# Kernel optimization log

Hardware: AMD Instinct MI355X
Metric: run time of the kernel (lower is better)

## Reference

```python
import jax, jax.numpy as jnp
import numpy as np

SIZE = 7
SIGMA = 1.5
K1 = 0.01
K2 = 0.03
DATA_RANGE = 2.0
NP_ = SIZE * SIZE
COV_NORM = NP_ / (NP_ - 1)
PAD = SIZE // 2


def _gaussian_window(size=SIZE, sigma=SIGMA, channels=1):
    x = np.arange(size) - size // 2
    g = np.exp(-x**2 / (2.0 * sigma**2))[None, :]
    g = (g.T @ g)
    g = g / g.sum()
    w = np.tile(g[None, None], (channels, 1, 1, 1))  # [C,1,size,size]
    return jnp.asarray(w, dtype=jnp.float32)


def _dwconv(x, w):
    # depthwise conv2d, zero padding PAD, stride 1; x: [N,C,H,W], w: [C,1,k,k]
    c = x.shape[1]
    return jax.lax.conv_general_dilated(
        x, w, window_strides=(1, 1), padding=[(PAD, PAD), (PAD, PAD)],
        dimension_numbers=('NCHW', 'OIHW', 'NCHW'), feature_group_count=c)


def setup_inputs() -> dict:
    key = jax.random.key(0)
    k1, k2 = jax.random.split(key)
    X = jax.random.uniform(k1, (64, 1, 320, 320), dtype=jnp.float32)
    Y = jax.random.uniform(k2, (64, 1, 320, 320), dtype=jnp.float32)
    window = _gaussian_window()
    return {"X": X, "Y": Y, "window": window}


def reference(X, Y, window):
    C1 = (K1 * DATA_RANGE) ** 2
    C2 = (K2 * DATA_RANGE) ** 2
    mux = _dwconv(X, window)
    muy = _dwconv(Y, window)
    mux_sq = mux * mux
    muy_sq = muy * muy
    muxy = mux * muy
    sigmax_sq = (_dwconv(X * X, window) - mux_sq) * COV_NORM
    sigmay_sq = (_dwconv(Y * Y, window) - muy_sq) * COV_NORM
    sigmaxy = (_dwconv(X * Y, window) - muxy) * COV_NORM
    ssim_map = ((2 * muxy + C1) * (2 * sigmaxy + C2)) / \
               ((mux_sq + muy_sq + C1) * (sigmax_sq + sigmay_sq + C2))
    return 1.0 - ssim_map.mean()
```

## Files before the change

kernel.cpp:

```cpp
#include <hip/hip_runtime.h>
#include <math.h>


#define WI 320
#define HI 320
#define NI 64
#define TWO 58
#define GXD 6
#define RPB 32
#define ITERS 8
#define GYD 10
#define NBLK (GXD * GYD * NI)
#define NPIX ((double)NI * WI * HI)

typedef float v4 __attribute__((ext_vector_type(4)));

struct W7 { float w[7]; };

__device__ __forceinline__ void issue_loads(
    const float* __restrict__ Xn, const float* __restrict__ Yn,
    int gx, bool xok, int ybase, float (&xr)[10], float (&yr)[10])
{
#pragma unroll
    for (int j = 0; j < 10; ++j) {
        const int gy  = ybase + j;
        const bool ok = xok && ((unsigned)gy < (unsigned)HI);
        float xv = 0.f, yv = 0.f;
        if (ok) { const int idx = gy * WI + gx; xv = Xn[idx]; yv = Yn[idx]; }
        xr[j] = xv; yr[j] = yv;
    }
}

__device__ __forceinline__ float compute_strip(
    const W7& wv, float* __restrict__ vb,
    const float (&xr)[10], const float (&yr)[10], int lane, int maxc)
{
    float acc[5][4];
#pragma unroll
    for (int ch = 0; ch < 5; ++ch)
#pragma unroll
        for (int r = 0; r < 4; ++r) acc[ch][r] = 0.f;
#pragma unroll
    for (int j = 0; j < 10; ++j) {
        const float xv = xr[j], yv = yr[j];
        const float pxx = xv * xv, pyy = yv * yv, pxy = xv * yv;
#pragma unroll
        for (int r = 0; r < 4; ++r) {
            const int d = j - r;
            if (d >= 0 && d < 7) {
                const float w = wv.w[d];
                acc[0][r] += w * xv;
                acc[1][r] += w * yv;
                acc[2][r] += w * pxx;
                acc[3][r] += w * pyy;
                acc[4][r] += w * pxy;
            }
        }
    }
#pragma unroll
    for (int ch = 0; ch < 5; ++ch)
#pragma unroll
        for (int r = 0; r < 4; ++r)
            vb[ch * 256 + r * 64 + lane] = acc[ch][r];

    __builtin_amdgcn_wave_barrier();

    const int row = lane >> 4;
    const int xg  = (lane & 15) << 2;
    const float C1 = 0.0004f, C2 = 0.0036f, COVN = 49.f / 48.f;

    float m[4][5];
#pragma unroll
    for (int j = 0; j < 4; ++j)
#pragma unroll
        for (int ch = 0; ch < 5; ++ch) m[j][ch] = 0.f;
#pragma unroll
    for (int ch = 0; ch < 5; ++ch) {
        const v4* p = (const v4*)&vb[ch * 256 + row * 64 + xg];
        v4 a = p[0], b = p[1], c = p[2];
        float f[12] = {a.x,a.y,a.z,a.w, b.x,b.y,b.z,b.w, c.x,c.y,c.z,c.w};
#pragma unroll
        for (int j = 0; j < 4; ++j) {
            float s = 0.f;
#pragma unroll
            for (int d = 0; d < 7; ++d) s += wv.w[d] * f[j + d];
            m[j][ch] = s;
        }
    }
    float lsum = 0.f;
#pragma unroll
    for (int j = 0; j < 4; ++j) {
        const float mx = m[j][0], my = m[j][1];
        const float mxsq = mx * mx;
        const float mysq = my * my;
        const float mxy  = mx * my;
        const float vx   = (m[j][2] - mxsq) * COVN;
        const float vy   = (m[j][3] - mysq) * COVN;
        const float vxy  = (m[j][4] - mxy)  * COVN;
        const float num  = (2.f * mxy + C1) * (2.f * vxy + C2);
        const float den  = (mxsq + mysq + C1) * (vx + vy + C2);
        lsum += (xg + j < maxc) ? num * __builtin_amdgcn_rcpf(den) : 0.f;
    }
    return lsum;
}

__global__ __launch_bounds__(64) void ssim_kernel(
    const float* __restrict__ X, const float* __restrict__ Y,
    W7 wv, float* __restrict__ partial)
{
    __shared__ __align__(16) float vbuf[5 * 4 * 64 + 16];

    const int lane = threadIdx.x;
    const int x0   = blockIdx.x * TWO;
    const int y0   = blockIdx.y * RPB;
    const float* __restrict__ Xn = X + (size_t)blockIdx.z * (WI * HI);
    const float* __restrict__ Yn = Y + (size_t)blockIdx.z * (WI * HI);

    const int  gx   = x0 + lane - 3;
    const bool xok  = (unsigned)gx < (unsigned)WI;
    const int  maxc = (x0 + TWO <= WI) ? TWO : (WI - x0);

    float ax[10], ay[10], bx[10], by[10];
    issue_loads(Xn, Yn, gx, xok, y0 - 3, ax, ay);

    float lsum = 0.f;
#pragma unroll 1
    for (int ii = 0; ii < ITERS; ii += 2) {
        issue_loads(Xn, Yn, gx, xok, y0 + 4 * (ii + 1) - 3, bx, by);
        lsum += compute_strip(wv, vbuf, ax, ay, lane, maxc);
        if (ii + 2 < ITERS)
            issue_loads(Xn, Yn, gx, xok, y0 + 4 * (ii + 2) - 3, ax, ay);
        lsum += compute_strip(wv, vbuf, bx, by, lane, maxc);
    }

#pragma unroll
    for (int off = 32; off > 0; off >>= 1)
        lsum += __shfl_down(lsum, off, 64);
    if (lane == 0) {
        const int bid = (blockIdx.z * GYD + blockIdx.y) * GXD + blockIdx.x;
        partial[bid] = lsum;
    }
}

__global__ __launch_bounds__(256) void ssim_finalize(
    const float* __restrict__ partial, float* __restrict__ out)
{
    __shared__ double ws[4];
    const int tid = threadIdx.x;
    double s = 0.0;
    for (int i = tid; i < NBLK; i += 256) s += (double)partial[i];
#pragma unroll
    for (int off = 32; off > 0; off >>= 1)
        s += __shfl_down(s, off, 64);
    if ((tid & 63) == 0) ws[tid >> 6] = s;
    __syncthreads();
    if (tid == 0)
        out[0] = (float)(1.0 - ((ws[0] + ws[1]) + (ws[2] + ws[3])) / NPIX);
}

extern "C" void kernel_launch(void* const* d_in, const int* in_sizes, int n_in,
                              void* d_out, int out_size, void* d_ws, size_t ws_size,
                              hipStream_t stream) {
    const float* X = (const float*)d_in[0];
    const float* Y = (const float*)d_in[1];
    W7 wv;
    {
        double g[7], s = 0.0;
        for (int i = 0; i < 7; ++i) {
            double x = (double)(i - 3);
            g[i] = exp(-(x * x) / (2.0 * 1.5 * 1.5));
            s += g[i];
        }
        for (int i = 0; i < 7; ++i) wv.w[i] = (float)(g[i] / s);
    }

    float* partial = (float*)d_ws;

    dim3 grid(GXD, GYD, NI);
    ssim_kernel<<<grid, 64, 0, stream>>>(X, Y, wv, partial);
    ssim_finalize<<<1, 256, 0, stream>>>(partial, (float*)d_out);
}
```

Before: 112.7 us.

## Use sliding 14-row register window with 8-row strips and two waves per block

Replaces the 4-row strips, which reload 10 rows each, with 8-row strips that keep a sliding 14-row register window, so only 8 new rows are loaded per strip instead of recomputing a 6-row halo. Values are packed as float2 so paired X/Y math can use packed ops. LDS now holds three regions with padded strides for the horizontal pass. Each lane computes 8 output columns instead of 4. Blocks become two waves covering 64 rows, which changes the grid and the partial-sum count. The cost is higher register pressure from the larger window and accumulators, and less explicit prefetch overlap than the previous double-buffered loads.

```diff
diff --git a/kernel.cpp b/kernel.cpp
--- a/kernel.cpp
+++ b/kernel.cpp
@@ -7,137 +7,171 @@
 #define NI 64
 #define TWO 58
 #define GXD 6
-#define RPB 32
-#define ITERS 8
-#define GYD 10
+#define SROWS 32
+#define ITERS 4
+#define WPB 2
+#define RPB (WPB * SROWS)
+#define GYD (HI / RPB)
 #define NBLK (GXD * GYD * NI)
+#define NPART (NBLK * WPB)
 #define NPIX ((double)NI * WI * HI)
 
+#define MU_OFF 0
+#define SQ_OFF 1088
+#define XY_OFF 2176
+#define WAVE_LDS 2752
+
+typedef float v2 __attribute__((ext_vector_type(2)));
 typedef float v4 __attribute__((ext_vector_type(4)));
 
 struct W7 { float w[7]; };
 
-__device__ __forceinline__ void issue_loads(
-    const float* __restrict__ Xn, const float* __restrict__ Yn,
-    int gx, bool xok, int ybase, float (&xr)[10], float (&yr)[10])
-{
-#pragma unroll
-    for (int j = 0; j < 10; ++j) {
-        const int gy  = ybase + j;
-        const bool ok = xok && ((unsigned)gy < (unsigned)HI);
-        float xv = 0.f, yv = 0.f;
-        if (ok) { const int idx = gy * WI + gx; xv = Xn[idx]; yv = Yn[idx]; }
-        xr[j] = xv; yr[j] = yv;
-    }
-}
-
-__device__ __forceinline__ float compute_strip(
-    const W7& wv, float* __restrict__ vb,
-    const float (&xr)[10], const float (&yr)[10], int lane, int maxc)
-{
-    float acc[5][4];
-#pragma unroll
-    for (int ch = 0; ch < 5; ++ch)
-#pragma unroll
-        for (int r = 0; r < 4; ++r) acc[ch][r] = 0.f;
-#pragma unroll
-    for (int j = 0; j < 10; ++j) {
-        const float xv = xr[j], yv = yr[j];
-        const float pxx = xv * xv, pyy = yv * yv, pxy = xv * yv;
-#pragma unroll
-        for (int r = 0; r < 4; ++r) {
-            const int d = j - r;
-            if (d >= 0 && d < 7) {
-                const float w = wv.w[d];
-                acc[0][r] += w * xv;
-                acc[1][r] += w * yv;
-                acc[2][r] += w * pxx;
-                acc[3][r] += w * pyy;
-                acc[4][r] += w * pxy;
-            }
-        }
-    }
-#pragma unroll
-    for (int ch = 0; ch < 5; ++ch)
-#pragma unroll
-        for (int r = 0; r < 4; ++r)
-            vb[ch * 256 + r * 64 + lane] = acc[ch][r];
-
-    __builtin_amdgcn_wave_barrier();
-
-    const int row = lane >> 4;
-    const int xg  = (lane & 15) << 2;
-    const float C1 = 0.0004f, C2 = 0.0036f, COVN = 49.f / 48.f;
-
-    float m[4][5];
-#pragma unroll
-    for (int j = 0; j < 4; ++j)
-#pragma unroll
-        for (int ch = 0; ch < 5; ++ch) m[j][ch] = 0.f;
-#pragma unroll
-    for (int ch = 0; ch < 5; ++ch) {
-        const v4* p = (const v4*)&vb[ch * 256 + row * 64 + xg];
-        v4 a = p[0], b = p[1], c = p[2];
-        float f[12] = {a.x,a.y,a.z,a.w, b.x,b.y,b.z,b.w, c.x,c.y,c.z,c.w};
-#pragma unroll
-        for (int j = 0; j < 4; ++j) {
-            float s = 0.f;
-#pragma unroll
-            for (int d = 0; d < 7; ++d) s += wv.w[d] * f[j + d];
-            m[j][ch] = s;
-        }
-    }
-    float lsum = 0.f;
-#pragma unroll
-    for (int j = 0; j < 4; ++j) {
-        const float mx = m[j][0], my = m[j][1];
-        const float mxsq = mx * mx;
-        const float mysq = my * my;
-        const float mxy  = mx * my;
-        const float vx   = (m[j][2] - mxsq) * COVN;
-        const float vy   = (m[j][3] - mysq) * COVN;
-        const float vxy  = (m[j][4] - mxy)  * COVN;
-        const float num  = (2.f * mxy + C1) * (2.f * vxy + C2);
-        const float den  = (mxsq + mysq + C1) * (vx + vy + C2);
-        lsum += (xg + j < maxc) ? num * __builtin_amdgcn_rcpf(den) : 0.f;
-    }
-    return lsum;
-}
-
-__global__ __launch_bounds__(64) void ssim_kernel(
+__device__ __forceinline__ v2 pget(const v4* t, int p) {
+    v4 q = t[p >> 1];
+    return (p & 1) ? (v2){q.z, q.w} : (v2){q.x, q.y};
+}
+__device__ __forceinline__ float sget(const v4* t, int p) {
+    v4 q = t[p >> 2];
+    switch (p & 3) { case 0: return q.x; case 1: return q.y; case 2: return q.z; default: return q.w; }
+}
+
+__global__ __launch_bounds__(WPB * 64) void ssim_kernel(
     const float* __restrict__ X, const float* __restrict__ Y,
     W7 wv, float* __restrict__ partial)
 {
-    __shared__ __align__(16) float vbuf[5 * 4 * 64 + 16];
-
-    const int lane = threadIdx.x;
-    const int x0   = blockIdx.x * TWO;
-    const int y0   = blockIdx.y * RPB;
+    __shared__ __align__(16) float lds_all[WPB * WAVE_LDS + 16];
+
+    const int tid  = threadIdx.x;
+    const int lane = tid & 63;
+    const int wid  = tid >> 6;
+    float* lds = lds_all + wid * WAVE_LDS;
+
+    const int x0 = blockIdx.x * TWO;
+    const int y0 = blockIdx.y * RPB + wid * SROWS;
     const float* __restrict__ Xn = X + (size_t)blockIdx.z * (WI * HI);
     const float* __restrict__ Yn = Y + (size_t)blockIdx.z * (WI * HI);
 
     const int  gx   = x0 + lane - 3;
     const bool xok  = (unsigned)gx < (unsigned)WI;
-    const int  maxc = (x0 + TWO <= WI) ? TWO : (WI - x0);
-
-    float ax[10], ay[10], bx[10], by[10];
-    issue_loads(Xn, Yn, gx, xok, y0 - 3, ax, ay);
+    const int  gxc  = min(max(gx, 0), WI - 1);
+    const int  maxc = min(TWO, WI - x0);
+
+    v2 win[14];
+#pragma unroll
+    for (int k = 0; k < 6; ++k) {
+        const int gy  = y0 - 3 + k;
+        const bool ok = xok && ((unsigned)gy < (unsigned)HI);
+        const int gyc = min(max(gy, 0), HI - 1);
+        const size_t idx = (size_t)gyc * WI + gxc;
+        v2 t; t.x = Xn[idx]; t.y = Yn[idx];
+        win[k] = ok ? t : (v2){0.f, 0.f};
+    }
+
+    const float C1 = 0.0004f, C2 = 0.0036f, COVN = 49.f / 48.f;
+    const int row = lane >> 3;
+    const int g   = lane & 7;
 
     float lsum = 0.f;
 #pragma unroll 1
-    for (int ii = 0; ii < ITERS; ii += 2) {
-        issue_loads(Xn, Yn, gx, xok, y0 + 4 * (ii + 1) - 3, bx, by);
-        lsum += compute_strip(wv, vbuf, ax, ay, lane, maxc);
-        if (ii + 2 < ITERS)
-            issue_loads(Xn, Yn, gx, xok, y0 + 4 * (ii + 2) - 3, ax, ay);
-        lsum += compute_strip(wv, vbuf, bx, by, lane, maxc);
+    for (int it = 0; it < ITERS; ++it) {
+        const int base_row = y0 + it * 8;
+
+#pragma unroll
+        for (int k = 0; k < 8; ++k) {
+            const int gy  = base_row + 3 + k;
+            const bool ok = xok && ((unsigned)gy < (unsigned)HI);
+            const int gyc = min(max(gy, 0), HI - 1);
+            const size_t idx = (size_t)gyc * WI + gxc;
+            v2 t; t.x = Xn[idx]; t.y = Yn[idx];
+            win[6 + k] = ok ? t : (v2){0.f, 0.f};
+        }
+
+        v2 amu[8], asq[8]; float axy[8];
+#pragma unroll
+        for (int r = 0; r < 8; ++r) { amu[r] = (v2){0.f,0.f}; asq[r] = (v2){0.f,0.f}; axy[r] = 0.f; }
+#pragma unroll
+        for (int k = 0; k < 14; ++k) {
+            const v2 v   = win[k];
+            const v2 sq  = v * v;
+            const float pxy = v.x * v.y;
+#pragma unroll
+            for (int r = 0; r < 8; ++r) {
+                const int d = k - r;
+                if (d >= 0 && d < 7) {
+                    const float w = wv.w[d];
+                    amu[r] += w * v;
+                    asq[r] += w * sq;
+                    axy[r] += w * pxy;
+                }
+            }
+        }
+
+#pragma unroll
+        for (int r = 0; r < 8; ++r) {
+            *(v2*)&lds[MU_OFF + r * 136 + 2 * lane] = amu[r];
+            *(v2*)&lds[SQ_OFF + r * 136 + 2 * lane] = asq[r];
+            lds[XY_OFF + r * 68 + lane] = axy[r];
+        }
+        __builtin_amdgcn_wave_barrier();
+
+        v2 mmu[8], msq[8]; float mxy[8];
+#pragma unroll
+        for (int j = 0; j < 8; ++j) { mmu[j] = (v2){0.f,0.f}; msq[j] = (v2){0.f,0.f}; mxy[j] = 0.f; }
+        {
+            v4 t[8];
+#pragma unroll
+            for (int q = 0; q < 8; ++q)
+                t[q] = *(const v4*)&lds[MU_OFF + row * 136 + 16 * g + 4 * q];
+#pragma unroll
+            for (int j = 0; j < 8; ++j)
+#pragma unroll
+                for (int d = 0; d < 7; ++d)
+                    mmu[j] += wv.w[d] * pget(t, j + d);
+        }
+        {
+            v4 t[8];
+#pragma unroll
+            for (int q = 0; q < 8; ++q)
+                t[q] = *(const v4*)&lds[SQ_OFF + row * 136 + 16 * g + 4 * q];
+#pragma unroll
+            for (int j = 0; j < 8; ++j)
+#pragma unroll
+                for (int d = 0; d < 7; ++d)
+                    msq[j] += wv.w[d] * pget(t, j + d);
+        }
+        {
+            v4 t[4];
+#pragma unroll
+            for (int q = 0; q < 4; ++q)
+                t[q] = *(const v4*)&lds[XY_OFF + row * 68 + 8 * g + 4 * q];
+#pragma unroll
+            for (int j = 0; j < 8; ++j)
+#pragma unroll
+                for (int d = 0; d < 7; ++d)
+                    mxy[j] += wv.w[d] * sget(t, j + d);
+        }
+
+#pragma unroll
+        for (int j = 0; j < 8; ++j) {
+            const v2 mu    = mmu[j];
+            const v2 musq  = mu * mu;
+            const float pm = mu.x * mu.y;
+            const v2 sig   = (msq[j] - musq) * COVN;
+            const float vxy = (mxy[j] - pm) * COVN;
+            const float num = (2.f * pm + C1) * (2.f * vxy + C2);
+            const float den = (musq.x + musq.y + C1) * (sig.x + sig.y + C2);
+            lsum += (8 * g + j < maxc) ? num * __builtin_amdgcn_rcpf(den) : 0.f;
+        }
+
+#pragma unroll
+        for (int k = 0; k < 6; ++k) win[k] = win[k + 8];
     }
 
 #pragma unroll
     for (int off = 32; off > 0; off >>= 1)
         lsum += __shfl_down(lsum, off, 64);
     if (lane == 0) {
-        const int bid = (blockIdx.z * GYD + blockIdx.y) * GXD + blockIdx.x;
+        const int bid = ((blockIdx.z * GYD + blockIdx.y) * GXD + blockIdx.x) * WPB + wid;
         partial[bid] = lsum;
     }
 }
@@ -148,7 +182,7 @@
     __shared__ double ws[4];
     const int tid = threadIdx.x;
     double s = 0.0;
-    for (int i = tid; i < NBLK; i += 256) s += (double)partial[i];
+    for (int i = tid; i < NPART; i += 256) s += (double)partial[i];
 #pragma unroll
     for (int off = 32; off > 0; off >>= 1)
         s += __shfl_down(s, off, 64);
@@ -165,18 +199,18 @@
     const float* Y = (const float*)d_in[1];
     W7 wv;
     {
-        double g[7], s = 0.0;
+        double gk[7], s = 0.0;
         for (int i = 0; i < 7; ++i) {
             double x = (double)(i - 3);
-            g[i] = exp(-(x * x) / (2.0 * 1.5 * 1.5));
-            s += g[i];
-        }
-        for (int i = 0; i < 7; ++i) wv.w[i] = (float)(g[i] / s);
+            gk[i] = exp(-(x * x) / (2.0 * 1.5 * 1.5));
+            s += gk[i];
+        }
+        for (int i = 0; i < 7; ++i) wv.w[i] = (float)(gk[i] / s);
     }
 
     float* partial = (float*)d_ws;
 
     dim3 grid(GXD, GYD, NI);
-    ssim_kernel<<<grid, 64, 0, stream>>>(X, Y, wv, partial);
+    ssim_kernel<<<grid, WPB * 64, 0, stream>>>(X, Y, wv, partial);
     ssim_finalize<<<1, 256, 0, stream>>>(partial, (float*)d_out);
 }
```

After: 110.8 us. Within noise of the previous version (-1.7%).
